# Optimization experiments

Hardware: AMD Instinct MI355X
Metric: run time of the kernel (lower is better)

Reference implementation:

```python
import jax, jax.numpy as jnp
import numpy as np

D_MODEL = 1024
N_HEADS = 16
D_K = D_MODEL // N_HEADS
SEQ = 2048
BATCH = 4


def setup_inputs() -> dict:
    key = jax.random.key(0)
    ks = jax.random.split(key, 11)
    s = 0.02
    inp = {
        'query': jax.random.normal(ks[0], (SEQ, BATCH, D_MODEL), jnp.float32),
        'key': jax.random.normal(ks[1], (SEQ, BATCH, D_MODEL), jnp.float32),
        'value': jax.random.normal(ks[2], (SEQ, BATCH, D_MODEL), jnp.float32),
        'Wq': jax.random.normal(ks[3], (D_MODEL, D_MODEL), jnp.float32) * s,
        'bq': jnp.zeros((D_MODEL,), jnp.float32),
        'Wk': jax.random.normal(ks[4], (D_MODEL, D_MODEL), jnp.float32) * s,
        'bk': jnp.zeros((D_MODEL,), jnp.float32),
        'Wv': jax.random.normal(ks[5], (D_MODEL, D_MODEL), jnp.float32) * s,
        'bv': jnp.zeros((D_MODEL,), jnp.float32),
        'Wo': jax.random.normal(ks[6], (D_MODEL, D_MODEL), jnp.float32) * s,
        'bo': jnp.zeros((D_MODEL,), jnp.float32),
    }
    return inp


def reference(query, key, value, Wq, bq, Wk, bk, Wv, bv, Wo, bo):
    # inputs are [S, B, D]; module transposes to batch-first
    q_in = jnp.swapaxes(query, 0, 1)  # [B, S, D]
    k_in = jnp.swapaxes(key, 0, 1)
    v_in = jnp.swapaxes(value, 0, 1)
    B, S, _ = q_in.shape
    # torch Linear: x @ W.T + b
    q = (q_in @ Wq.T + bq).reshape(B, S, N_HEADS, D_K)
    k = (k_in @ Wk.T + bk).reshape(B, S, N_HEADS, D_K)
    v = (v_in @ Wv.T + bv).reshape(B, S, N_HEADS, D_K)
    scale = jnp.sqrt(jnp.float32(D_K))
    scores = jnp.einsum('bqhd,bkhd->bhqk', q, k) / scale  # [B, H, S, S]
    attn = jax.nn.softmax(scores, axis=-1)
    # dropout is identity in eval / p=0
    context = jnp.einsum('bhqk,bkhd->bqhd', attn, v).reshape(B, S, D_MODEL)
    out = context @ Wo.T + bo  # [B, S, D]
    return jnp.swapaxes(out, 0, 1)  # back to [S, B, D]
```

## Files before the change

### kernel.cpp

```cpp
#include <hip/hip_runtime.h>
#include <math.h>

typedef unsigned short u16;
typedef unsigned int   u32;
typedef float f32x4 __attribute__((ext_vector_type(4)));
typedef __bf16 bf16x8 __attribute__((ext_vector_type(8)));
typedef __bf16 bf16x2 __attribute__((ext_vector_type(2)));

#define SEQ   2048
#define BATCH 4
#define NH    16
#define DK    64
#define DM    1024
#define MTOT  (SEQ*BATCH)
#define SCL_QK 0.18033688011116016f

static __device__ __forceinline__ u16 f2bf(float f) {
  __bf16 h = (__bf16)f;
  return __builtin_bit_cast(u16, h);
}
static __device__ __forceinline__ u32 pk2(float a, float b) {
  bf16x2 t = {(__bf16)a, (__bf16)b};
  return __builtin_bit_cast(u32, t);
}

typedef __attribute__((address_space(1))) const void g1_t;
typedef __attribute__((address_space(3))) void l3_t;
static __device__ __forceinline__ void gload16(const void* g, void* l) {
  __builtin_amdgcn_global_load_lds((g1_t*)g, (l3_t*)l, 16, 0, 0);
}

static __device__ __forceinline__ void cast8(const float* __restrict__ src,
                                             u16* __restrict__ dst, int i) {
  float4 a = ((const float4*)src)[2 * i];
  float4 b = ((const float4*)src)[2 * i + 1];
  uint4 r;
  r.x = pk2(a.x, a.y); r.y = pk2(a.z, a.w);
  r.z = pk2(b.x, b.y); r.w = pk2(b.z, b.w);
  ((uint4*)dst)[i] = r;
}

__global__ __launch_bounds__(256)
void cast_bf16(const float* __restrict__ src, u16* __restrict__ dst, int n8) {
  int i = blockIdx.x * 256 + threadIdx.x;
  if (i < n8) cast8(src, dst, i);
}

__global__ __launch_bounds__(256)
void cast_w(const float* __restrict__ Wq, const float* __restrict__ Wk,
            const float* __restrict__ Wv, const float* __restrict__ Wo,
            u16* __restrict__ w3, u16* __restrict__ wo_c) {
  int bid = blockIdx.x;
  int t = bid >> 9, idx = bid & 511;
  const float* src = (t == 0) ? Wq : (t == 1) ? Wk : (t == 2) ? Wv : Wo;
  u16* dst = (t < 3) ? (w3 + (size_t)t * DM * DM) : wo_c;
  cast8(src, dst, idx * 256 + threadIdx.x);
}

__global__ __launch_bounds__(256)
void cast_all(const float* __restrict__ q, const float* __restrict__ k,
              const float* __restrict__ v,
              const float* __restrict__ Wq, const float* __restrict__ Wk,
              const float* __restrict__ Wv, const float* __restrict__ Wo,
              u16* __restrict__ in_c, u16* __restrict__ w3, u16* __restrict__ wo_c) {
  int bid = blockIdx.x;
  const float* src; u16* dst; int idx;
  if (bid < 12288) {
    int t = bid >> 12; idx = bid & 4095;
    src = (t == 0) ? q : (t == 1) ? k : v;
    dst = in_c + (size_t)t * MTOT * DM;
  } else {
    int wb = bid - 12288;
    int t = wb >> 9; idx = wb & 511;
    src = (t == 0) ? Wq : (t == 1) ? Wk : (t == 2) ? Wv : Wo;
    dst = (t < 3) ? (w3 + (size_t)t * DM * DM) : wo_c;
  }
  cast8(src, dst, idx * 256 + threadIdx.x);
}

template<int OGEMM>
__global__ __launch_bounds__(256, 4)
void gemm_k(const u16* __restrict__ a0, const u16* __restrict__ a1,
            const u16* __restrict__ a2, const u16* __restrict__ w3,
            const float* __restrict__ b0, const float* __restrict__ b1,
            const float* __restrict__ b2,
            u16* __restrict__ o0, u16* __restrict__ o1, u16* __restrict__ o2,
            float* __restrict__ o3, int seg_base)
{
  constexpr int BM = 128, BN = 128, BK = 32;
  __shared__ u16 As[BM * BK];
  __shared__ u16 Bs[BN * BK];

  const int seg = OGEMM ? 0 : (seg_base + (int)(blockIdx.x >> 3));
  const int n0  = OGEMM ? blockIdx.x * BN : (blockIdx.x & 7) * BN;
  const int m0  = blockIdx.y * BM;
  const u16* A = OGEMM ? a0 : (seg == 0 ? a0 : seg == 1 ? a1 : a2);
  const u16* W = OGEMM ? w3 : (w3 + (size_t)seg * DM * DM);
  const float* bias = OGEMM ? b0 : (seg == 0 ? b0 : seg == 1 ? b1 : b2);

  const int tid  = threadIdx.x;
  const int w    = tid >> 6;
  const int lane = tid & 63;
  const int quad = lane >> 4;
  const int l15  = lane & 15;
  const int wm = (w >> 1) * 64;
  const int wn = (w & 1) * 64;

  size_t aoff[2], woff[2];
  for (int p = 0; p < 2; p++) {
    int row = w * 32 + p * 16 + (lane >> 2);
    int gm = m0 + row;
    if (OGEMM) {
      aoff[p] = (size_t)gm * DM + (lane & 3) * 8;
    } else {
      int bb = gm >> 11, s = gm & (SEQ - 1);
      aoff[p] = (size_t)(s * BATCH + bb) * DM + (lane & 3) * 8;
    }
    woff[p] = (size_t)(n0 + row) * DM + (lane & 3) * 8;
  }

  f32x4 zero4 = {0.f, 0.f, 0.f, 0.f};
  f32x4 acc[4][4];
  for (int i = 0; i < 4; i++)
    for (int j = 0; j < 4; j++)
      acc[i][j] = zero4;

  for (int k0 = 0; k0 < DM; k0 += BK) {
    for (int p = 0; p < 2; p++) {
      gload16(A + aoff[p] + k0, &As[(w * 32 + p * 16) * BK]);
      gload16(W + woff[p] + k0, &Bs[(w * 32 + p * 16) * BK]);
    }
    __syncthreads();
    bf16x8 af[4], bfr[4];
    for (int i = 0; i < 4; i++)
      af[i] = *(const bf16x8*)&As[(wm + i * 16 + l15) * BK + quad * 8];
    for (int j = 0; j < 4; j++)
      bfr[j] = *(const bf16x8*)&Bs[(wn + j * 16 + l15) * BK + quad * 8];
    for (int i = 0; i < 4; i++)
      for (int j = 0; j < 4; j++)
        acc[i][j] = __builtin_amdgcn_mfma_f32_16x16x32_bf16(af[i], bfr[j], acc[i][j], 0, 0, 0);
    __syncthreads();
  }

  for (int j = 0; j < 4; j++) {
    int gn = n0 + wn + j * 16 + l15;
    float bv = bias[gn];
    int h = gn >> 6, dk = gn & 63;
    for (int i = 0; i < 4; i++) {
      int gmb = m0 + wm + i * 16 + quad * 4;
      for (int r = 0; r < 4; r++) {
        int gm = gmb + r;
        float val = acc[i][j][r] + bv;
        int bb = gm >> 11, s = gm & (SEQ - 1);
        if (OGEMM) {
          o3[(size_t)(s * BATCH + bb) * DM + gn] = val;
        } else if (seg == 0) {
          o0[((size_t)(bb * NH + h) * SEQ + s) * DK + dk] = f2bf(val * SCL_QK);
        } else if (seg == 1) {
          o1[((size_t)(bb * NH + h) * SEQ + s) * DK + dk] = f2bf(val);
        } else {
          o2[((size_t)(bb * NH + h) * DK + dk) * SEQ + s] = f2bf(val);
        }
      }
    }
  }
}

__global__ __launch_bounds__(256, 4)
void attn3(const u16* __restrict__ Q, const u16* __restrict__ K,
           const u16* __restrict__ VT, u16* __restrict__ ctx)
{
  __shared__ u16 Ks[64 * 64];
  __shared__ u16 Vs[64 * 64];
  __shared__ u16 Ps[4][32][72];

  const int bh = blockIdx.x;
  const int qt = blockIdx.y;
  const int b  = bh >> 4, h = bh & 15;
  const int tid  = threadIdx.x;
  const int w    = tid >> 6;
  const int lane = tid & 63;
  const int quad = lane >> 4;
  const int l15  = lane & 15;

  const u16* Qb = Q  + (size_t)bh * SEQ * DK;
  const u16* Kb = K  + (size_t)bh * SEQ * DK;
  const u16* Vb = VT + (size_t)bh * DK * SEQ;

  const int qbase = qt * 128 + w * 32;
  bf16x8 qf[2][2];
  for (int qh = 0; qh < 2; qh++)
    for (int kc = 0; kc < 2; kc++)
      qf[qh][kc] = *(const bf16x8*)&Qb[(size_t)(qbase + qh * 16 + l15) * DK + kc * 32 + quad * 8];

  float lsum[2] = {0.f, 0.f};
  f32x4 zero4 = {0.f, 0.f, 0.f, 0.f};
  f32x4 ot[2][4];
  for (int qh = 0; qh < 2; qh++)
    for (int fn = 0; fn < 4; fn++) ot[qh][fn] = zero4;

  const int r0 = tid >> 3;
  const int sw = (tid & 7) ^ (r0 & 7);
  const int s3 = l15 & 7;
  const int c0 = ((0 + quad) ^ s3) * 8;
  const int c1 = ((4 + quad) ^ s3) * 8;

  for (int kb = 0; kb < SEQ / 64; kb++) {
    __syncthreads();
    for (int p = 0; p < 2; p++) {
      int row = p * 32 + r0;
      gload16(&Kb[(size_t)(kb * 64 + row) * DK + sw * 8], &Ks[(p * 32 + w * 8) * 64]);
      gload16(&Vb[(size_t)row * SEQ + kb * 64 + sw * 8], &Vs[(p * 32 + w * 8) * 64]);
    }
    __syncthreads();

    f32x4 st[2][4];
    for (int qh = 0; qh < 2; qh++)
      for (int fn = 0; fn < 4; fn++) st[qh][fn] = zero4;
    for (int kc = 0; kc < 2; kc++)
      for (int fn = 0; fn < 4; fn++) {
        bf16x8 kf = *(const bf16x8*)&Ks[(fn * 16 + l15) * 64 + (kc ? c1 : c0)];
        for (int qh = 0; qh < 2; qh++)
          st[qh][fn] = __builtin_amdgcn_mfma_f32_16x16x32_bf16(kf, qf[qh][kc], st[qh][fn], 0, 0, 0);
      }

    for (int qh = 0; qh < 2; qh++) {
      float part = 0.f;
      for (int fn = 0; fn < 4; fn++)
        for (int r = 0; r < 4; r++) {
          float p = exp2f(st[qh][fn][r]);
          st[qh][fn][r] = p;
          part += p;
        }
      lsum[qh] += part;
    }

    for (int qh = 0; qh < 2; qh++)
      for (int fn = 0; fn < 4; fn++) {
        uint2 pr;
        pr.x = pk2(st[qh][fn][0], st[qh][fn][1]);
        pr.y = pk2(st[qh][fn][2], st[qh][fn][3]);
        *(uint2*)&Ps[w][qh * 16 + l15][fn * 16 + quad * 4] = pr;
      }

    for (int kc = 0; kc < 2; kc++) {
      bf16x8 pf[2];
      for (int qh = 0; qh < 2; qh++)
        pf[qh] = *(const bf16x8*)&Ps[w][qh * 16 + l15][kc * 32 + quad * 8];
      for (int fn = 0; fn < 4; fn++) {
        bf16x8 vf = *(const bf16x8*)&Vs[(fn * 16 + l15) * 64 + (kc ? c1 : c0)];
        for (int qh = 0; qh < 2; qh++)
          ot[qh][fn] = __builtin_amdgcn_mfma_f32_16x16x32_bf16(vf, pf[qh], ot[qh][fn], 0, 0, 0);
      }
    }
  }

  for (int qh = 0; qh < 2; qh++) {
    float l = lsum[qh];
    l += __shfl_xor(l, 16);
    l += __shfl_xor(l, 32);
    float inv = 1.0f / l;
    int qg = qbase + qh * 16 + l15;
    for (int fn = 0; fn < 4; fn++) {
      uint2 pr;
      pr.x = pk2(ot[qh][fn][0] * inv, ot[qh][fn][1] * inv);
      pr.y = pk2(ot[qh][fn][2] * inv, ot[qh][fn][3] * inv);
      *(uint2*)&ctx[((size_t)(b * SEQ + qg)) * DM + h * DK + fn * 16 + quad * 4] = pr;
    }
  }
}

extern "C" void kernel_launch(void* const* d_in, const int* in_sizes, int n_in,
                              void* d_out, int out_size, void* d_ws, size_t ws_size,
                              hipStream_t stream)
{
  const float* q  = (const float*)d_in[0];
  const float* k  = (const float*)d_in[1];
  const float* v  = (const float*)d_in[2];
  const float* Wq = (const float*)d_in[3];
  const float* bq = (const float*)d_in[4];
  const float* Wk = (const float*)d_in[5];
  const float* bk = (const float*)d_in[6];
  const float* Wv = (const float*)d_in[7];
  const float* bv = (const float*)d_in[8];
  const float* Wo = (const float*)d_in[9];
  const float* bo = (const float*)d_in[10];

  const size_t SZ_IN  = (size_t)MTOT * DM;
  const size_t SZ_W   = (size_t)DM * DM;
  const size_t NEED_FUSED = (3 * SZ_IN + 3 * SZ_W + SZ_W + 3 * SZ_IN) * 2;

  dim3 cblk(256);
  dim3 ggq(24, 64);
  dim3 ggs(8, 64);

  if (ws_size >= NEED_FUSED) {
    u16* in_c  = (u16*)d_ws;
    u16* w3    = in_c + 3 * SZ_IN;
    u16* wo_c  = w3   + 3 * SZ_W;
    u16* q_ws  = wo_c + SZ_W;
    u16* k_ws  = q_ws + SZ_IN;
    u16* vt_ws = k_ws + SZ_IN;
    u16* ctx   = in_c;

    cast_all<<<14336, cblk, 0, stream>>>(q, k, v, Wq, Wk, Wv, Wo, in_c, w3, wo_c);
    gemm_k<0><<<ggq, cblk, 0, stream>>>(in_c, in_c + SZ_IN, in_c + 2 * SZ_IN, w3,
                                        bq, bk, bv, q_ws, k_ws, vt_ws, nullptr, 0);
    attn3<<<dim3(BATCH * NH, SEQ / 128), cblk, 0, stream>>>(q_ws, k_ws, vt_ws, ctx);
    gemm_k<1><<<ggs, cblk, 0, stream>>>(ctx, ctx, ctx, wo_c,
                                        bo, bo, bo, nullptr, nullptr, nullptr,
                                        (float*)d_out, 0);
  } else {
    u16* in_c  = (u16*)d_ws;
    u16* w3    = in_c + SZ_IN;
    u16* wo_c  = w3   + 3 * SZ_W;
    u16* q_ws  = wo_c + SZ_W;
    u16* k_ws  = q_ws + SZ_IN;
    u16* vt_ws = k_ws + SZ_IN;
    u16* ctx   = in_c;

    const int NA8 = MTOT * DM / 8;
    cast_w<<<2048, cblk, 0, stream>>>(Wq, Wk, Wv, Wo, w3, wo_c);
    cast_bf16<<<NA8 / 256, cblk, 0, stream>>>(q, in_c, NA8);
    gemm_k<0><<<ggs, cblk, 0, stream>>>(in_c, in_c, in_c, w3, bq, bk, bv,
                                        q_ws, k_ws, vt_ws, nullptr, 0);
    cast_bf16<<<NA8 / 256, cblk, 0, stream>>>(k, in_c, NA8);
    gemm_k<0><<<ggs, cblk, 0, stream>>>(in_c, in_c, in_c, w3, bq, bk, bv,
                                        q_ws, k_ws, vt_ws, nullptr, 1);
    cast_bf16<<<NA8 / 256, cblk, 0, stream>>>(v, in_c, NA8);
    gemm_k<0><<<ggs, cblk, 0, stream>>>(in_c, in_c, in_c, w3, bq, bk, bv,
                                        q_ws, k_ws, vt_ws, nullptr, 2);
    attn3<<<dim3(BATCH * NH, SEQ / 128), cblk, 0, stream>>>(q_ws, k_ws, vt_ws, ctx);
    gemm_k<1><<<ggs, cblk, 0, stream>>>(ctx, ctx, ctx, wo_c,
                                        bo, bo, bo, nullptr, nullptr, nullptr,
                                        (float*)d_out, 0);
  }
}
```

Measured before the change: 411.9 us.

## Double-buffer K/V tiles and keep P in registers with 32x32 MFMA

```diff
diff --git a/kernel.cpp b/kernel.cpp
--- a/kernel.cpp
+++ b/kernel.cpp
@@ -3,7 +3,8 @@
 
 typedef unsigned short u16;
 typedef unsigned int   u32;
-typedef float f32x4 __attribute__((ext_vector_type(4)));
+typedef float f32x4  __attribute__((ext_vector_type(4)));
+typedef float f32x16 __attribute__((ext_vector_type(16)));
 typedef __bf16 bf16x8 __attribute__((ext_vector_type(8)));
 typedef __bf16 bf16x2 __attribute__((ext_vector_type(2)));
 
@@ -14,6 +15,12 @@
 #define DM    1024
 #define MTOT  (SEQ*BATCH)
 #define SCL_QK 0.18033688011116016f
+
+#if __has_builtin(__builtin_amdgcn_exp2f)
+#define EXP2(x) __builtin_amdgcn_exp2f(x)
+#else
+#define EXP2(x) exp2f(x)
+#endif
 
 static __device__ __forceinline__ u16 f2bf(float f) {
   __bf16 h = (__bf16)f;
@@ -170,9 +177,8 @@
 void attn3(const u16* __restrict__ Q, const u16* __restrict__ K,
            const u16* __restrict__ VT, u16* __restrict__ ctx)
 {
-  __shared__ u16 Ks[64 * 64];
-  __shared__ u16 Vs[64 * 64];
-  __shared__ u16 Ps[4][32][72];
+  __shared__ u16 Ks[2][64 * 64];
+  __shared__ u16 Vs[2][64 * 64];
 
   const int bh = blockIdx.x;
   const int qt = blockIdx.y;
@@ -180,94 +186,124 @@
   const int tid  = threadIdx.x;
   const int w    = tid >> 6;
   const int lane = tid & 63;
-  const int quad = lane >> 4;
-  const int l15  = lane & 15;
+  const int l31  = lane & 31;
+  const int hi   = lane >> 5;
 
   const u16* Qb = Q  + (size_t)bh * SEQ * DK;
   const u16* Kb = K  + (size_t)bh * SEQ * DK;
   const u16* Vb = VT + (size_t)bh * DK * SEQ;
 
   const int qbase = qt * 128 + w * 32;
-  bf16x8 qf[2][2];
-  for (int qh = 0; qh < 2; qh++)
-    for (int kc = 0; kc < 2; kc++)
-      qf[qh][kc] = *(const bf16x8*)&Qb[(size_t)(qbase + qh * 16 + l15) * DK + kc * 32 + quad * 8];
-
-  float lsum[2] = {0.f, 0.f};
-  f32x4 zero4 = {0.f, 0.f, 0.f, 0.f};
-  f32x4 ot[2][4];
-  for (int qh = 0; qh < 2; qh++)
-    for (int fn = 0; fn < 4; fn++) ot[qh][fn] = zero4;
+  const int qrow  = qbase + l31;
+
+  bf16x8 qf[4];
+#pragma unroll
+  for (int ks = 0; ks < 4; ks++)
+    qf[ks] = *(const bf16x8*)&Qb[(size_t)qrow * DK + ks * 16 + hi * 8];
 
   const int r0 = tid >> 3;
   const int sw = (tid & 7) ^ (r0 & 7);
-  const int s3 = l15 & 7;
-  const int c0 = ((0 + quad) ^ s3) * 8;
-  const int c1 = ((4 + quad) ^ s3) * 8;
+
+#define STAGE(kbb, bufi) do {                                                       \
+    _Pragma("unroll")                                                               \
+    for (int p = 0; p < 2; p++) {                                                   \
+      int row = p * 32 + r0;                                                        \
+      gload16(&Kb[(size_t)((kbb) * 64 + row) * DK + sw * 8],                        \
+              &Ks[bufi][(p * 32 + w * 8) * 64]);                                    \
+      gload16(&Vb[(size_t)row * SEQ + (kbb) * 64 + sw * 8],                         \
+              &Vs[bufi][(p * 32 + w * 8) * 64]);                                    \
+    }                                                                               \
+  } while (0)
+
+  f32x16 z16;
+#pragma unroll
+  for (int i = 0; i < 16; i++) z16[i] = 0.f;
+
+  f32x16 ot0 = z16, ot1 = z16;
+  float2 ls2 = {0.f, 0.f};
+
+  STAGE(0, 0);
+  __syncthreads();
 
   for (int kb = 0; kb < SEQ / 64; kb++) {
+    const int buf = kb & 1;
+    if (kb + 1 < SEQ / 64) STAGE(kb + 1, buf ^ 1);
+
+    const u16* KsB = &Ks[buf][0];
+    const u16* VsB = &Vs[buf][0];
+
+    f32x16 sa0 = z16, sa1 = z16;
+#pragma unroll
+    for (int ks = 0; ks < 4; ks++) {
+      const int g0 = ((ks * 2 + hi) ^ (l31 & 7)) * 8;
+      bf16x8 kf0 = *(const bf16x8*)&KsB[l31 * 64 + g0];
+      bf16x8 kf1 = *(const bf16x8*)&KsB[(32 + l31) * 64 + g0];
+      sa0 = __builtin_amdgcn_mfma_f32_32x32x16_bf16(kf0, qf[ks], sa0, 0, 0, 0);
+      sa1 = __builtin_amdgcn_mfma_f32_32x32x16_bf16(kf1, qf[ks], sa1, 0, 0, 0);
+    }
+
+    u32 wp[8];
+
+#define SOFTMAX_BLK(SA) do {                                                        \
+    _Pragma("unroll")                                                               \
+    for (int g = 0; g < 8; g++) {                                                   \
+      float pa = EXP2(SA[2 * g]);                                                   \
+      float pb = EXP2(SA[2 * g + 1]);                                               \
+      ls2.x += pa; ls2.y += pb;                                                     \
+      wp[g] = pk2(pa, pb);                                                          \
+    }                                                                               \
+  } while (0)
+
+#define PVSTEP(KSB, KSL) do {                                                       \
+    u32 a0 = wp[(KSB) * 4 + 0], a1 = wp[(KSB) * 4 + 1];                             \
+    u32 a2 = wp[(KSB) * 4 + 2], a3 = wp[(KSB) * 4 + 3];                             \
+    u32 s0 = hi ? a0 : a2, s1 = hi ? a1 : a3;                                       \
+    u32 x0 = (u32)__shfl_xor((int)s0, 32);                                          \
+    u32 x1 = (u32)__shfl_xor((int)s1, 32);                                          \
+    uint4 pw;                                                                       \
+    pw.x = hi ? x0 : a0; pw.y = hi ? x1 : a1;                                       \
+    pw.z = hi ? a2 : x0; pw.w = hi ? a3 : x1;                                       \
+    bf16x8 pf = __builtin_bit_cast(bf16x8, pw);                                     \
+    const int gg = (((KSL) * 2 + hi) ^ (l31 & 7)) * 8;                              \
+    bf16x8 vf0 = *(const bf16x8*)&VsB[l31 * 64 + gg];                               \
+    bf16x8 vf1 = *(const bf16x8*)&VsB[(32 + l31) * 64 + gg];                        \
+    ot0 = __builtin_amdgcn_mfma_f32_32x32x16_bf16(vf0, pf, ot0, 0, 0, 0);           \
+    ot1 = __builtin_amdgcn_mfma_f32_32x32x16_bf16(vf1, pf, ot1, 0, 0, 0);           \
+  } while (0)
+
+    SOFTMAX_BLK(sa0);
+    PVSTEP(0, 0);
+    PVSTEP(1, 1);
+    SOFTMAX_BLK(sa1);
+    PVSTEP(0, 2);
+    PVSTEP(1, 3);
+
     __syncthreads();
-    for (int p = 0; p < 2; p++) {
-      int row = p * 32 + r0;
-      gload16(&Kb[(size_t)(kb * 64 + row) * DK + sw * 8], &Ks[(p * 32 + w * 8) * 64]);
-      gload16(&Vb[(size_t)row * SEQ + kb * 64 + sw * 8], &Vs[(p * 32 + w * 8) * 64]);
-    }
-    __syncthreads();
-
-    f32x4 st[2][4];
-    for (int qh = 0; qh < 2; qh++)
-      for (int fn = 0; fn < 4; fn++) st[qh][fn] = zero4;
-    for (int kc = 0; kc < 2; kc++)
-      for (int fn = 0; fn < 4; fn++) {
-        bf16x8 kf = *(const bf16x8*)&Ks[(fn * 16 + l15) * 64 + (kc ? c1 : c0)];
-        for (int qh = 0; qh < 2; qh++)
-          st[qh][fn] = __builtin_amdgcn_mfma_f32_16x16x32_bf16(kf, qf[qh][kc], st[qh][fn], 0, 0, 0);
-      }
-
-    for (int qh = 0; qh < 2; qh++) {
-      float part = 0.f;
-      for (int fn = 0; fn < 4; fn++)
-        for (int r = 0; r < 4; r++) {
-          float p = exp2f(st[qh][fn][r]);
-          st[qh][fn][r] = p;
-          part += p;
-        }
-      lsum[qh] += part;
-    }
-
-    for (int qh = 0; qh < 2; qh++)
-      for (int fn = 0; fn < 4; fn++) {
-        uint2 pr;
-        pr.x = pk2(st[qh][fn][0], st[qh][fn][1]);
-        pr.y = pk2(st[qh][fn][2], st[qh][fn][3]);
-        *(uint2*)&Ps[w][qh * 16 + l15][fn * 16 + quad * 4] = pr;
-      }
-
-    for (int kc = 0; kc < 2; kc++) {
-      bf16x8 pf[2];
-      for (int qh = 0; qh < 2; qh++)
-        pf[qh] = *(const bf16x8*)&Ps[w][qh * 16 + l15][kc * 32 + quad * 8];
-      for (int fn = 0; fn < 4; fn++) {
-        bf16x8 vf = *(const bf16x8*)&Vs[(fn * 16 + l15) * 64 + (kc ? c1 : c0)];
-        for (int qh = 0; qh < 2; qh++)
-          ot[qh][fn] = __builtin_amdgcn_mfma_f32_16x16x32_bf16(vf, pf[qh], ot[qh][fn], 0, 0, 0);
-      }
-    }
-  }
-
-  for (int qh = 0; qh < 2; qh++) {
-    float l = lsum[qh];
-    l += __shfl_xor(l, 16);
-    l += __shfl_xor(l, 32);
-    float inv = 1.0f / l;
-    int qg = qbase + qh * 16 + l15;
-    for (int fn = 0; fn < 4; fn++) {
-      uint2 pr;
-      pr.x = pk2(ot[qh][fn][0] * inv, ot[qh][fn][1] * inv);
-      pr.y = pk2(ot[qh][fn][2] * inv, ot[qh][fn][3] * inv);
-      *(uint2*)&ctx[((size_t)(b * SEQ + qg)) * DM + h * DK + fn * 16 + quad * 4] = pr;
-    }
-  }
+  }
+
+  float ls = ls2.x + ls2.y;
+  ls += __shfl_xor(ls, 32);
+  float inv = 1.0f / ls;
+
+  u16* crow = ctx + ((size_t)(b * SEQ + qrow)) * DM + h * DK;
+
+#define STORE_BLK(OT, DKB) do {                                                     \
+    _Pragma("unroll")                                                               \
+    for (int t = 0; t < 4; t++) {                                                   \
+      uint2 pr;                                                                     \
+      pr.x = pk2(OT[4 * t + 0] * inv, OT[4 * t + 1] * inv);                         \
+      pr.y = pk2(OT[4 * t + 2] * inv, OT[4 * t + 3] * inv);                         \
+      *(uint2*)&crow[(DKB) * 32 + t * 8 + hi * 4] = pr;                             \
+    }                                                                               \
+  } while (0)
+
+  STORE_BLK(ot0, 0);
+  STORE_BLK(ot1, 1);
+
+#undef STAGE
+#undef SOFTMAX_BLK
+#undef PVSTEP
+#undef STORE_BLK
 }
 
 extern "C" void kernel_launch(void* const* d_in, const int* in_sizes, int n_in,
```

Result: faster. 384.9 us (-6.6%).
